# Kernel optimization log

Measured on AMD Instinct MI355X. Metric: run time of the kernel, lower is better.

## Reference

```python
import jax, jax.numpy as jnp
import numpy as np

B, D, LC, LQ = 64, 128, 1024, 128
NEG = -1e30


def setup_inputs() -> dict:
    key = jax.random.key(0)
    k1, k2, k3 = jax.random.split(key, 3)
    lim = float(np.sqrt(1.0 / D))
    return {
        "C": jax.random.normal(k1, (B, D, LC), dtype=jnp.float32),
        "Q": jax.random.normal(k2, (B, D, LQ), dtype=jnp.float32),
        "cmask": jnp.ones((B, LC), dtype=jnp.float32),
        "qmask": jnp.ones((B, LQ), dtype=jnp.float32),
        "w": jax.random.uniform(k3, (3 * D,), dtype=jnp.float32, minval=-lim, maxval=lim),
    }


def reference(C, Q, cmask, qmask, w):
    # C: [B, D, Lc], Q: [B, D, Lq] -> transpose to [B, L, D] as in the torch module
    Ct = jnp.swapaxes(C, 1, 2)  # [B, Lc, D]
    Qt = jnp.swapaxes(Q, 1, 2)  # [B, Lq, D]
    d = Ct.shape[-1]
    # Trilinear decomposition of the per-step concat([Qi, C, Q*C]) . w loop:
    # S[b,c,q] = Qt[b,q] . w_q + Ct[b,c] . w_c + (Ct[b,c] * w_m) . Qt[b,q]
    w_q, w_c, w_m = w[:d], w[d:2 * d], w[2 * d:]
    s_q = Qt @ w_q                                   # [B, Lq]
    s_c = Ct @ w_c                                   # [B, Lc]
    s_m = jnp.einsum("bcd,bqd->bcq", Ct * w_m, Qt)   # [B, Lc, Lq]
    S = s_m + s_c[:, :, None] + s_q[:, None, :]      # [B, Lc, Lq]

    S1 = jax.nn.softmax(S + (1.0 - qmask)[:, None, :] * NEG, axis=2)
    S2 = jax.nn.softmax(S + (1.0 - cmask)[:, :, None] * NEG, axis=1)

    A = jnp.einsum("bcq,bqd->bcd", S1, Qt)           # [B, Lc, D]
    S12 = jnp.einsum("bcq,bkq->bck", S1, S2)         # [B, Lc, Lc]
    Bt = jnp.einsum("bck,bkd->bcd", S12, Ct)         # [B, Lc, D]

    out = jnp.concatenate([Ct, A, Ct * A, Ct * Bt], axis=2)  # [B, Lc, 4D]
    # dropout is identity in eval mode
    return jnp.swapaxes(out, 1, 2)                   # [B, 4D, Lc]
```

## Files before the change

kernel.cpp:

```cpp
#include <hip/hip_runtime.h>
#include <cstdint>
#include <cstddef>

#define B_  64
#define D_  128
#define LC_ 1024
#define LQ_ 128
#define NEGV (-1e30f)
#define NINF (-3.402823466e38f)

typedef short s16x8 __attribute__((ext_vector_type(8)));
typedef float f32x4 __attribute__((ext_vector_type(4)));

__device__ __forceinline__ unsigned short f2bf(float x) {
    union { float f; unsigned u; } v; v.f = x;
    unsigned r = v.u + 0x7fffu + ((v.u >> 16) & 1u);
    return (unsigned short)(r >> 16);
}

__global__ __launch_bounds__(256, 2) void k1(const float* __restrict__ C,
                                             const float* __restrict__ Q,
                                             const float* __restrict__ cmask,
                                             const float* __restrict__ qmask,
                                             const float* __restrict__ w,
                                             unsigned short* __restrict__ S1b,
                                             float* __restrict__ pmax_g,
                                             float* __restrict__ psum_g,
                                             float* __restrict__ T2p) {
    __shared__ unsigned short CW[128 * 136];
    __shared__ unsigned short QT[128 * 136];
    __shared__ float4 red4[8][32];
    __shared__ float wc_l[128], wm_l[128], cmv_l[128], qmv_l[128], sc_l[128], sq_l[128];

    int t = threadIdx.x;
    int b = blockIdx.y, ct = blockIdx.x, c0 = ct * 128;
    int g = t >> 5, c4 = t & 31;

    float4 v[16];
    {
        const float4* Cb = (const float4*)(C + (size_t)b * D_ * LC_ + c0);
#pragma unroll
        for (int j = 0; j < 16; j++) {
            int d = j * 8 + g;
            v[j] = Cb[(size_t)d * (LC_ / 4) + c4];
        }
    }
    float* wq_l = (float*)red4;
    if (t < 128) {
        wq_l[t] = w[t];
        wc_l[t] = w[D_ + t];
        wm_l[t] = w[2 * D_ + t];
        cmv_l[t] = (1.0f - cmask[b * LC_ + c0 + t]) * NEGV;
        qmv_l[t] = (1.0f - qmask[b * LQ_ + t]) * NEGV;
    }
    __syncthreads();

    {
        float* CWf = (float*)CW;
        int qq = t >> 1, ph = t & 1;
        float sqv = 0.f;
#pragma unroll
        for (int h = 0; h < 2; h++) {
#pragma unroll
            for (int j = 0; j < 8; j++) {
                int idx = j * 256 + t;
                int r = idx >> 5, cc = idx & 31;
                float4 qv = *(const float4*)&Q[((size_t)(b * D_ + h * 64 + r)) * LQ_ + cc * 4];
                *(float4*)&CWf[r * 132 + cc * 4] = qv;
            }
            __syncthreads();
            unsigned short u[32];
#pragma unroll
            for (int k = 0; k < 32; k++) {
                float val = CWf[(ph * 32 + k) * 132 + qq];
                sqv += val * wq_l[h * 64 + ph * 32 + k];
                u[k] = f2bf(val);
            }
#pragma unroll
            for (int k4 = 0; k4 < 8; k4++) {
                ushort4 o;
                o.x = u[k4 * 4 + 0]; o.y = u[k4 * 4 + 1];
                o.z = u[k4 * 4 + 2]; o.w = u[k4 * 4 + 3];
                *(ushort4*)&QT[qq * 136 + h * 64 + ph * 32 + k4 * 4] = o;
            }
            __syncthreads();
        }
        sqv += __shfl_xor(sqv, 1, 64);
        if (ph == 0) sq_l[qq] = sqv;
    }

    {
        float4 scp = {0.f, 0.f, 0.f, 0.f};
#pragma unroll
        for (int j = 0; j < 16; j++) {
            int d = j * 8 + g;
            float wcv = wc_l[d], wmv = wm_l[d];
            scp.x += v[j].x * wcv;
            scp.y += v[j].y * wcv;
            scp.z += v[j].z * wcv;
            scp.w += v[j].w * wcv;
            ushort4 o;
            o.x = f2bf(v[j].x * wmv);
            o.y = f2bf(v[j].y * wmv);
            o.z = f2bf(v[j].z * wmv);
            o.w = f2bf(v[j].w * wmv);
            *(ushort4*)&CW[d * 136 + ((c4 ^ (j & 7)) << 2)] = o;
        }
        red4[g][c4] = scp;
    }
    __syncthreads();
    if (t < 128) {
        float s = 0.f;
#pragma unroll
        for (int gg = 0; gg < 8; gg++) {
            const float* rp = (const float*)&red4[gg][t >> 2];
            s += rp[t & 3];
        }
        sc_l[t] = s;
    }
    __syncthreads();

    int wv = t >> 6, l = t & 63, quad = l >> 4, lp = l & 15;
    int w32 = wv * 32;
    f32x4 zero = {0.f, 0.f, 0.f, 0.f};
    f32x4 acc[2][8];
#pragma unroll
    for (int mc = 0; mc < 2; mc++)
#pragma unroll
        for (int qt = 0; qt < 8; qt++) acc[mc][qt] = zero;

#pragma unroll
    for (int ks = 0; ks < 4; ks++) {
        s16x8 a[2], bb[8];
        int x3 = (ks * 4 + quad) & 7;
#pragma unroll
        for (int mc = 0; mc < 2; mc++) {
            s16x8 av;
            int c = w32 + mc * 16 + lp;
            int cb = ((c >> 2) ^ x3) << 2, clo = c & 3;
#pragma unroll
            for (int e = 0; e < 8; e++)
                av[e] = (short)CW[(ks * 32 + quad * 8 + e) * 136 + cb + clo];
            a[mc] = av;
        }
#pragma unroll
        for (int qt = 0; qt < 8; qt++)
            bb[qt] = *(const s16x8*)&QT[(qt * 16 + lp) * 136 + ks * 32 + quad * 8];
#pragma unroll
        for (int mc = 0; mc < 2; mc++)
#pragma unroll
            for (int qt = 0; qt < 8; qt++)
                acc[mc][qt] = __builtin_amdgcn_mfma_f32_16x16x32_bf16(a[mc], bb[qt], acc[mc][qt], 0, 0, 0);
    }
#pragma unroll
    for (int mc = 0; mc < 2; mc++)
#pragma unroll
        for (int qt = 0; qt < 8; qt++)
#pragma unroll
            for (int i = 0; i < 4; i++)
                acc[mc][qt][i] += sc_l[w32 + mc * 16 + quad * 4 + i] + sq_l[qt * 16 + lp];

    float qmv_r[8];
#pragma unroll
    for (int qt = 0; qt < 8; qt++) qmv_r[qt] = qmv_l[qt * 16 + lp];
    float cmv_r[2][4];
#pragma unroll
    for (int mc = 0; mc < 2; mc++)
#pragma unroll
        for (int i = 0; i < 4; i++) cmv_r[mc][i] = cmv_l[w32 + mc * 16 + quad * 4 + i];

    float rm_r[2][4];
#pragma unroll
    for (int mc = 0; mc < 2; mc++)
#pragma unroll
        for (int i = 0; i < 4; i++) {
            float m = NINF;
#pragma unroll
            for (int qt = 0; qt < 8; qt++) m = fmaxf(m, acc[mc][qt][i] + qmv_r[qt]);
#pragma unroll
            for (int off = 1; off < 16; off <<= 1) m = fmaxf(m, __shfl_xor(m, off, 64));
            rm_r[mc][i] = m;
        }

    int chunk = ct * 4 + wv;
#pragma unroll
    for (int qt = 0; qt < 8; qt++) {
        float cm = NINF;
#pragma unroll
        for (int mc = 0; mc < 2; mc++)
#pragma unroll
            for (int i = 0; i < 4; i++) cm = fmaxf(cm, acc[mc][qt][i] + cmv_r[mc][i]);
        cm = fmaxf(cm, __shfl_xor(cm, 16, 64));
        cm = fmaxf(cm, __shfl_xor(cm, 32, 64));
        float cs = 0.f;
#pragma unroll
        for (int mc = 0; mc < 2; mc++)
#pragma unroll
            for (int i = 0; i < 4; i++) cs += __expf(acc[mc][qt][i] + cmv_r[mc][i] - cm);
        cs += __shfl_xor(cs, 16, 64);
        cs += __shfl_xor(cs, 32, 64);
        if (l < 16) {
            pmax_g[((size_t)(b * 32 + chunk)) * LQ_ + qt * 16 + lp] = cm;
            psum_g[((size_t)(b * 32 + chunk)) * LQ_ + qt * 16 + lp] = cs;
        }
    }

    float ri_r[2][4], gs_r[2][4];
#pragma unroll
    for (int mc = 0; mc < 2; mc++)
#pragma unroll
        for (int i = 0; i < 4; i++) {
            float s = 0.f;
#pragma unroll
            for (int qt = 0; qt < 8; qt++) {
                float e = __expf(acc[mc][qt][i] + qmv_r[qt] - rm_r[mc][i]);
                acc[mc][qt][i] = e;
                s += e;
            }
#pragma unroll
            for (int off = 1; off < 16; off <<= 1) s += __shfl_xor(s, off, 64);
            ri_r[mc][i] = 1.0f / s;
            gs_r[mc][i] = s * __expf(rm_r[mc][i] + cmv_r[mc][i]);
        }

    __syncthreads();
#pragma unroll
    for (int mc = 0; mc < 2; mc++)
#pragma unroll
        for (int qt = 0; qt < 8; qt++)
#pragma unroll
            for (int i = 0; i < 4; i++) {
                int row = w32 + mc * 16 + quad * 4 + i;
                int q = qt * 16 + lp;
                float s1 = acc[mc][qt][i] * ri_r[mc][i];
                CW[row * 136 + q] = f2bf(s1);
                QT[q * 136 + row] = f2bf(s1 * gs_r[mc][i]);
            }
    __syncthreads();

    {
        int row = t >> 1, qh = (t & 1) * 64;
        const uint4* src = (const uint4*)&CW[row * 136 + qh];
        uint4* dst = (uint4*)&S1b[((size_t)(b * LC_ + c0 + row)) * LQ_ + qh];
#pragma unroll
        for (int j = 0; j < 8; j++) dst[j] = src[j];
    }

    f32x4 acc2[2][8];
#pragma unroll
    for (int mc = 0; mc < 2; mc++)
#pragma unroll
        for (int nt = 0; nt < 8; nt++) acc2[mc][nt] = zero;
#pragma unroll
    for (int ks = 0; ks < 4; ks++) {
        s16x8 a2[2], bb[8];
#pragma unroll
        for (int m = 0; m < 2; m++) {
            int d = w32 + m * 16 + lp;
            const float4* p = (const float4*)&C[((size_t)(b * D_ + d)) * LC_ + c0 + ks * 32 + quad * 8];
            float4 v0 = p[0], v1 = p[1];
            unsigned short* pp = (unsigned short*)&a2[m];
            pp[0] = f2bf(v0.x); pp[1] = f2bf(v0.y); pp[2] = f2bf(v0.z); pp[3] = f2bf(v0.w);
            pp[4] = f2bf(v1.x); pp[5] = f2bf(v1.y); pp[6] = f2bf(v1.z); pp[7] = f2bf(v1.w);
        }
#pragma unroll
        for (int nt = 0; nt < 8; nt++)
            bb[nt] = *(const s16x8*)&QT[(nt * 16 + lp) * 136 + ks * 32 + quad * 8];
#pragma unroll
        for (int m = 0; m < 2; m++)
#pragma unroll
            for (int nt = 0; nt < 8; nt++)
                acc2[m][nt] = __builtin_amdgcn_mfma_f32_16x16x32_bf16(a2[m], bb[nt], acc2[m][nt], 0, 0, 0);
    }
    size_t base = ((size_t)(ct * B_ + b)) * ((size_t)D_ * LQ_);
#pragma unroll
    for (int mc = 0; mc < 2; mc++)
#pragma unroll
        for (int i = 0; i < 4; i++) {
            int d = w32 + mc * 16 + quad * 4 + i;
#pragma unroll
            for (int nt = 0; nt < 8; nt++)
                T2p[base + (size_t)d * LQ_ + nt * 16 + lp] = acc2[mc][nt][i];
        }
}

__global__ __launch_bounds__(256) void k2(const float* __restrict__ pmax_g,
                                          const float* __restrict__ psum_g,
                                          const float* __restrict__ T2p,
                                          unsigned short* __restrict__ T2b) {
    __shared__ float scale_l[128];
    int t = threadIdx.x;
    int bid = blockIdx.x;
    int b = bid >> 3, dc = bid & 7;
    if (t < 128) {
        float m = NINF;
        for (int j = 0; j < 32; j++)
            m = fmaxf(m, pmax_g[((size_t)(b * 32 + j)) * LQ_ + t]);
        float s = 0.f;
        for (int j = 0; j < 32; j++)
            s += psum_g[((size_t)(b * 32 + j)) * LQ_ + t] *
                 __expf(pmax_g[((size_t)(b * 32 + j)) * LQ_ + t] - m);
        scale_l[t] = __expf(-m) / s;
    }
    __syncthreads();
    int d = dc * 16 + (t >> 4), q8 = (t & 15) * 8;
    float a8[8] = {0.f, 0.f, 0.f, 0.f, 0.f, 0.f, 0.f, 0.f};
#pragma unroll
    for (int j = 0; j < 8; j++) {
        const float* p = &T2p[(((size_t)j * B_ + b) * D_ + d) * LQ_ + q8];
        float4 x0 = *(const float4*)p, x1 = *(const float4*)(p + 4);
        a8[0] += x0.x; a8[1] += x0.y; a8[2] += x0.z; a8[3] += x0.w;
        a8[4] += x1.x; a8[5] += x1.y; a8[6] += x1.z; a8[7] += x1.w;
    }
    ushort4 o0, o1;
    o0.x = f2bf(a8[0] * scale_l[q8 + 0]);
    o0.y = f2bf(a8[1] * scale_l[q8 + 1]);
    o0.z = f2bf(a8[2] * scale_l[q8 + 2]);
    o0.w = f2bf(a8[3] * scale_l[q8 + 3]);
    o1.x = f2bf(a8[4] * scale_l[q8 + 4]);
    o1.y = f2bf(a8[5] * scale_l[q8 + 5]);
    o1.z = f2bf(a8[6] * scale_l[q8 + 6]);
    o1.w = f2bf(a8[7] * scale_l[q8 + 7]);
    size_t tb = ((size_t)(b * D_ + d)) * LQ_ + q8;
    *(ushort4*)&T2b[tb] = o0;
    *(ushort4*)&T2b[tb + 4] = o1;
}

__global__ __launch_bounds__(256) void k3(const float* __restrict__ C,
                                          const float* __restrict__ Q,
                                          const unsigned short* __restrict__ T2b,
                                          const unsigned short* __restrict__ S1b,
                                          float* __restrict__ out) {
    int t = threadIdx.x;
    int b = blockIdx.y, c0 = blockIdx.x * 128;
    int wv = t >> 6, l = t & 63, quad = l >> 4, lp = l & 15;
    int w32 = wv * 32;
    f32x4 zero = {0.f, 0.f, 0.f, 0.f};
    f32x4 accA[2][8], accB[2][8];
#pragma unroll
    for (int mc = 0; mc < 2; mc++)
#pragma unroll
        for (int nt = 0; nt < 8; nt++) { accA[mc][nt] = zero; accB[mc][nt] = zero; }

#pragma unroll
    for (int ks = 0; ks < 4; ks++) {
        s16x8 aq[2], at[2], bb[8];
#pragma unroll
        for (int mc = 0; mc < 2; mc++) {
            int d = w32 + mc * 16 + lp;
            const float4* p = (const float4*)&Q[((size_t)(b * D_ + d)) * LQ_ + ks * 32 + quad * 8];
            float4 v0 = p[0], v1 = p[1];
            unsigned short* pp = (unsigned short*)&aq[mc];
            pp[0] = f2bf(v0.x); pp[1] = f2bf(v0.y); pp[2] = f2bf(v0.z); pp[3] = f2bf(v0.w);
            pp[4] = f2bf(v1.x); pp[5] = f2bf(v1.y); pp[6] = f2bf(v1.z); pp[7] = f2bf(v1.w);
            at[mc] = *(const s16x8*)&T2b[((size_t)(b * D_ + d)) * LQ_ + ks * 32 + quad * 8];
        }
#pragma unroll
        for (int nt = 0; nt < 8; nt++)
            bb[nt] = *(const s16x8*)&S1b[((size_t)(b * LC_ + c0 + nt * 16 + lp)) * LQ_ + ks * 32 + quad * 8];
#pragma unroll
        for (int mc = 0; mc < 2; mc++)
#pragma unroll
            for (int nt = 0; nt < 8; nt++) {
                accA[mc][nt] = __builtin_amdgcn_mfma_f32_16x16x32_bf16(aq[mc], bb[nt], accA[mc][nt], 0, 0, 0);
                accB[mc][nt] = __builtin_amdgcn_mfma_f32_16x16x32_bf16(at[mc], bb[nt], accB[mc][nt], 0, 0, 0);
            }
    }
    const size_t DL = (size_t)D_ * LC_;
#pragma unroll
    for (int mc = 0; mc < 2; mc++)
#pragma unroll
        for (int i = 0; i < 4; i++) {
            int d = w32 + mc * 16 + quad * 4 + i;
            const float* Crow = C + ((size_t)(b * D_ + d)) * LC_ + c0;
            size_t ob = ((size_t)(b * 4 * D_ + d)) * LC_ + c0;
#pragma unroll
            for (int nt = 0; nt < 8; nt++) {
                int c = nt * 16 + lp;
                float cv = Crow[c];
                float a = accA[mc][nt][i];
                float bt = accB[mc][nt][i];
                out[ob + c] = cv;
                out[ob + DL + c] = a;
                out[ob + 2 * DL + c] = cv * a;
                out[ob + 3 * DL + c] = cv * bt;
            }
        }
}

extern "C" void kernel_launch(void* const* d_in, const int* in_sizes, int n_in,
                              void* d_out, int out_size, void* d_ws, size_t ws_size,
                              hipStream_t stream) {
    const float* C     = (const float*)d_in[0];
    const float* Q     = (const float*)d_in[1];
    const float* cmask = (const float*)d_in[2];
    const float* qmask = (const float*)d_in[3];
    const float* w     = (const float*)d_in[4];
    float* out = (float*)d_out;

    unsigned short* us = (unsigned short*)d_ws;
    unsigned short* S1b = us;
    unsigned short* T2b = S1b + (size_t)B_ * LC_ * LQ_;
    float* fp = (float*)(T2b + (size_t)B_ * D_ * LQ_);
    float* T2p    = fp;
    float* pmax_g = T2p + (size_t)8 * B_ * D_ * LQ_;
    float* psum_g = pmax_g + (size_t)B_ * 32 * LQ_;

    k1<<<dim3(LC_ / 128, B_), 256, 0, stream>>>(C, Q, cmask, qmask, w,
                                                S1b, pmax_g, psum_g, T2p);
    k2<<<dim3(B_ * 8), 256, 0, stream>>>(pmax_g, psum_g, T2p, T2b);
    k3<<<dim3(LC_ / 128, B_), 256, 0, stream>>>(C, Q, T2b, S1b, out);
}
```

Before: 219.1 us.

## Reuse LDS C*w_m tile for T2 partials, store partials in bf16, nontemporal output

The second GEMM in k1 now reads its C operand from the bf16 C*w_m tile already in shared memory (XOR-swizzled) and rescales the result by 1/w_m, instead of reloading and converting C from global memory. The S1 tile is kept in registers and written back to shared memory afterwards. T2 partials are stored as bf16 in a q-major layout, and k2 transposes them through shared memory, which halves the partial traffic. k3 uses nontemporal stores for the large output. The 1/w_m trick loses the contribution of any d where w_m is zero and adds bf16 rounding error.

```diff
diff --git a/kernel.cpp b/kernel.cpp
--- a/kernel.cpp
+++ b/kernel.cpp
@@ -16,6 +16,9 @@
     union { float f; unsigned u; } v; v.f = x;
     unsigned r = v.u + 0x7fffu + ((v.u >> 16) & 1u);
     return (unsigned short)(r >> 16);
+}
+__device__ __forceinline__ float bf2f(unsigned short u) {
+    union { unsigned u; float f; } v; v.u = ((unsigned)u) << 16; return v.f;
 }
 
 __global__ __launch_bounds__(256, 2) void k1(const float* __restrict__ C,
@@ -26,11 +29,11 @@
                                              unsigned short* __restrict__ S1b,
                                              float* __restrict__ pmax_g,
                                              float* __restrict__ psum_g,
-                                             float* __restrict__ T2p) {
+                                             unsigned short* __restrict__ T2pb) {
     __shared__ unsigned short CW[128 * 136];
     __shared__ unsigned short QT[128 * 136];
     __shared__ float4 red4[8][32];
-    __shared__ float wc_l[128], wm_l[128], cmv_l[128], qmv_l[128], sc_l[128], sq_l[128];
+    __shared__ float wc_l[128], wm_l[128], rwm_l[128], cmv_l[128], qmv_l[128], sc_l[128], sq_l[128];
 
     int t = threadIdx.x;
     int b = blockIdx.y, ct = blockIdx.x, c0 = ct * 128;
@@ -47,9 +50,11 @@
     }
     float* wq_l = (float*)red4;
     if (t < 128) {
+        float wmv = w[2 * D_ + t];
         wq_l[t] = w[t];
         wc_l[t] = w[D_ + t];
-        wm_l[t] = w[2 * D_ + t];
+        wm_l[t] = wmv;
+        rwm_l[t] = (wmv != 0.0f) ? (1.0f / wmv) : 0.0f;
         cmv_l[t] = (1.0f - cmask[b * LC_ + c0 + t]) * NEGV;
         qmv_l[t] = (1.0f - qmask[b * LQ_ + t]) * NEGV;
     }
@@ -223,21 +228,85 @@
             gs_r[mc][i] = s * __expf(rm_r[mc][i] + cmv_r[mc][i]);
         }
 
-    __syncthreads();
-#pragma unroll
-    for (int mc = 0; mc < 2; mc++)
-#pragma unroll
-        for (int qt = 0; qt < 8; qt++)
+    unsigned s1pk[2][8][2];
+    __syncthreads();
+#pragma unroll
+    for (int mc = 0; mc < 2; mc++)
+#pragma unroll
+        for (int qt = 0; qt < 8; qt++) {
+            unsigned short u[4];
 #pragma unroll
             for (int i = 0; i < 4; i++) {
                 int row = w32 + mc * 16 + quad * 4 + i;
                 int q = qt * 16 + lp;
                 float s1 = acc[mc][qt][i] * ri_r[mc][i];
-                CW[row * 136 + q] = f2bf(s1);
+                u[i] = f2bf(s1);
                 QT[q * 136 + row] = f2bf(s1 * gs_r[mc][i]);
             }
-    __syncthreads();
-
+            s1pk[mc][qt][0] = (unsigned)u[0] | ((unsigned)u[1] << 16);
+            s1pk[mc][qt][1] = (unsigned)u[2] | ((unsigned)u[3] << 16);
+        }
+    __syncthreads();
+
+    f32x4 acc2[2][8];
+#pragma unroll
+    for (int mc = 0; mc < 2; mc++)
+#pragma unroll
+        for (int nt = 0; nt < 8; nt++) acc2[mc][nt] = zero;
+#pragma unroll
+    for (int ks = 0; ks < 4; ks++) {
+        s16x8 a2[2], bb[8];
+#pragma unroll
+        for (int m = 0; m < 2; m++) {
+            int d = w32 + m * 16 + lp;
+            int xd = (d >> 3) & 7;
+            int cg = ks * 8 + quad * 2;
+            union { s16x8 vv; uint2 u2[2]; } A;
+            A.u2[0] = *(const uint2*)&CW[d * 136 + ((cg ^ xd) << 2)];
+            A.u2[1] = *(const uint2*)&CW[d * 136 + (((cg + 1) ^ xd) << 2)];
+            a2[m] = A.vv;
+        }
+#pragma unroll
+        for (int nt = 0; nt < 8; nt++)
+            bb[nt] = *(const s16x8*)&QT[(nt * 16 + lp) * 136 + ks * 32 + quad * 8];
+#pragma unroll
+        for (int m = 0; m < 2; m++)
+#pragma unroll
+            for (int nt = 0; nt < 8; nt++)
+                acc2[m][nt] = __builtin_amdgcn_mfma_f32_16x16x32_bf16(a2[m], bb[nt], acc2[m][nt], 0, 0, 0);
+    }
+    {
+        size_t baseq = ((size_t)(ct * B_ + b)) * LQ_;
+#pragma unroll
+        for (int mc = 0; mc < 2; mc++) {
+            int d0 = w32 + mc * 16 + quad * 4;
+            float r0 = rwm_l[d0], r1 = rwm_l[d0 + 1], r2 = rwm_l[d0 + 2], r3 = rwm_l[d0 + 3];
+#pragma unroll
+            for (int nt = 0; nt < 8; nt++) {
+                int q = nt * 16 + lp;
+                ushort4 o;
+                o.x = f2bf(acc2[mc][nt][0] * r0);
+                o.y = f2bf(acc2[mc][nt][1] * r1);
+                o.z = f2bf(acc2[mc][nt][2] * r2);
+                o.w = f2bf(acc2[mc][nt][3] * r3);
+                *(ushort4*)&T2pb[(baseq + q) * D_ + d0] = o;
+            }
+        }
+    }
+
+    __syncthreads();
+#pragma unroll
+    for (int mc = 0; mc < 2; mc++)
+#pragma unroll
+        for (int qt = 0; qt < 8; qt++) {
+            int row0 = w32 + mc * 16 + quad * 4;
+            int q = qt * 16 + lp;
+            CW[(row0 + 0) * 136 + q] = (unsigned short)(s1pk[mc][qt][0] & 0xffffu);
+            CW[(row0 + 1) * 136 + q] = (unsigned short)(s1pk[mc][qt][0] >> 16);
+            CW[(row0 + 2) * 136 + q] = (unsigned short)(s1pk[mc][qt][1] & 0xffffu);
+            CW[(row0 + 3) * 136 + q] = (unsigned short)(s1pk[mc][qt][1] >> 16);
+        }
+    __syncthreads();
     {
         int row = t >> 1, qh = (t & 1) * 64;
         const uint4* src = (const uint4*)&CW[row * 136 + qh];
@@ -245,50 +314,14 @@
 #pragma unroll
         for (int j = 0; j < 8; j++) dst[j] = src[j];
     }
-
-    f32x4 acc2[2][8];
-#pragma unroll
-    for (int mc = 0; mc < 2; mc++)
-#pragma unroll
-        for (int nt = 0; nt < 8; nt++) acc2[mc][nt] = zero;
-#pragma unroll
-    for (int ks = 0; ks < 4; ks++) {
-        s16x8 a2[2], bb[8];
-#pragma unroll
-        for (int m = 0; m < 2; m++) {
-            int d = w32 + m * 16 + lp;
-            const float4* p = (const float4*)&C[((size_t)(b * D_ + d)) * LC_ + c0 + ks * 32 + quad * 8];
-            float4 v0 = p[0], v1 = p[1];
-            unsigned short* pp = (unsigned short*)&a2[m];
-            pp[0] = f2bf(v0.x); pp[1] = f2bf(v0.y); pp[2] = f2bf(v0.z); pp[3] = f2bf(v0.w);
-            pp[4] = f2bf(v1.x); pp[5] = f2bf(v1.y); pp[6] = f2bf(v1.z); pp[7] = f2bf(v1.w);
-        }
-#pragma unroll
-        for (int nt = 0; nt < 8; nt++)
-            bb[nt] = *(const s16x8*)&QT[(nt * 16 + lp) * 136 + ks * 32 + quad * 8];
-#pragma unroll
-        for (int m = 0; m < 2; m++)
-#pragma unroll
-            for (int nt = 0; nt < 8; nt++)
-                acc2[m][nt] = __builtin_amdgcn_mfma_f32_16x16x32_bf16(a2[m], bb[nt], acc2[m][nt], 0, 0, 0);
-    }
-    size_t base = ((size_t)(ct * B_ + b)) * ((size_t)D_ * LQ_);
-#pragma unroll
-    for (int mc = 0; mc < 2; mc++)
-#pragma unroll
-        for (int i = 0; i < 4; i++) {
-            int d = w32 + mc * 16 + quad * 4 + i;
-#pragma unroll
-            for (int nt = 0; nt < 8; nt++)
-                T2p[base + (size_t)d * LQ_ + nt * 16 + lp] = acc2[mc][nt][i];
-        }
 }
 
 __global__ __launch_bounds__(256) void k2(const float* __restrict__ pmax_g,
                                           const float* __restrict__ psum_g,
-                                          const float* __restrict__ T2p,
+                                          const unsigned short* __restrict__ T2pb,
                                           unsigned short* __restrict__ T2b) {
     __shared__ float scale_l[128];
+    __shared__ float trans[16][132];
     int t = threadIdx.x;
     int bid = blockIdx.x;
     int b = bid >> 3, dc = bid & 7;
@@ -303,27 +336,32 @@
         scale_l[t] = __expf(-m) / s;
     }
     __syncthreads();
-    int d = dc * 16 + (t >> 4), q8 = (t & 15) * 8;
-    float a8[8] = {0.f, 0.f, 0.f, 0.f, 0.f, 0.f, 0.f, 0.f};
-#pragma unroll
-    for (int j = 0; j < 8; j++) {
-        const float* p = &T2p[(((size_t)j * B_ + b) * D_ + d) * LQ_ + q8];
-        float4 x0 = *(const float4*)p, x1 = *(const float4*)(p + 4);
-        a8[0] += x0.x; a8[1] += x0.y; a8[2] += x0.z; a8[3] += x0.w;
-        a8[4] += x1.x; a8[5] += x1.y; a8[6] += x1.z; a8[7] += x1.w;
-    }
-    ushort4 o0, o1;
-    o0.x = f2bf(a8[0] * scale_l[q8 + 0]);
-    o0.y = f2bf(a8[1] * scale_l[q8 + 1]);
-    o0.z = f2bf(a8[2] * scale_l[q8 + 2]);
-    o0.w = f2bf(a8[3] * scale_l[q8 + 3]);
-    o1.x = f2bf(a8[4] * scale_l[q8 + 4]);
-    o1.y = f2bf(a8[5] * scale_l[q8 + 5]);
-    o1.z = f2bf(a8[6] * scale_l[q8 + 6]);
-    o1.w = f2bf(a8[7] * scale_l[q8 + 7]);
-    size_t tb = ((size_t)(b * D_ + d)) * LQ_ + q8;
-    *(ushort4*)&T2b[tb] = o0;
-    *(ushort4*)&T2b[tb + 4] = o1;
+    {
+        int q = t >> 1, dh = t & 1;
+        float a8[8] = {0.f, 0.f, 0.f, 0.f, 0.f, 0.f, 0.f, 0.f};
+#pragma unroll
+        for (int j = 0; j < 8; j++) {
+            const ushort4* p = (const ushort4*)&T2pb[(((size_t)j * B_ + b) * LQ_ + q) * D_ + dc * 16 + dh * 8];
+            ushort4 x0 = p[0], x1 = p[1];
+            a8[0] += bf2f(x0.x); a8[1] += bf2f(x0.y); a8[2] += bf2f(x0.z); a8[3] += bf2f(x0.w);
+            a8[4] += bf2f(x1.x); a8[5] += bf2f(x1.y); a8[6] += bf2f(x1.z); a8[7] += bf2f(x1.w);
+        }
+        float sc = scale_l[q];
+#pragma unroll
+        for (int k = 0; k < 8; k++) trans[dh * 8 + k][q] = a8[k] * sc;
+    }
+    __syncthreads();
+    {
+        int dl = t >> 4, q8 = (t & 15) * 8;
+        f32x4 v0 = *(const f32x4*)&trans[dl][q8];
+        f32x4 v1 = *(const f32x4*)&trans[dl][q8 + 4];
+        ushort4 o0, o1;
+        o0.x = f2bf(v0[0]); o0.y = f2bf(v0[1]); o0.z = f2bf(v0[2]); o0.w = f2bf(v0[3]);
+        o1.x = f2bf(v1[0]); o1.y = f2bf(v1[1]); o1.z = f2bf(v1[2]); o1.w = f2bf(v1[3]);
+        size_t tb = ((size_t)(b * D_ + dc * 16 + dl)) * LQ_ + q8;
+        *(ushort4*)&T2b[tb] = o0;
+        *(ushort4*)&T2b[tb + 4] = o1;
+    }
 }
 
 __global__ __launch_bounds__(256) void k3(const float* __restrict__ C,
@@ -380,10 +418,10 @@
                 float cv = Crow[c];
                 float a = accA[mc][nt][i];
                 float bt = accB[mc][nt][i];
-                out[ob + c] = cv;
-                out[ob + DL + c] = a;
-                out[ob + 2 * DL + c] = cv * a;
-                out[ob + 3 * DL + c] = cv * bt;
+                __builtin_nontemporal_store(cv, &out[ob + c]);
+                __builtin_nontemporal_store(a, &out[ob + DL + c]);
+                __builtin_nontemporal_store(cv * a, &out[ob + 2 * DL + c]);
+                __builtin_nontemporal_store(cv * bt, &out[ob + 3 * DL + c]);
             }
         }
 }
@@ -399,15 +437,15 @@
     float* out = (float*)d_out;
 
     unsigned short* us = (unsigned short*)d_ws;
-    unsigned short* S1b = us;
-    unsigned short* T2b = S1b + (size_t)B_ * LC_ * LQ_;
-    float* fp = (float*)(T2b + (size_t)B_ * D_ * LQ_);
-    float* T2p    = fp;
-    float* pmax_g = T2p + (size_t)8 * B_ * D_ * LQ_;
+    unsigned short* S1b  = us;
+    unsigned short* T2b  = S1b + (size_t)B_ * LC_ * LQ_;
+    unsigned short* T2pb = T2b + (size_t)B_ * D_ * LQ_;
+    float* fp = (float*)(T2pb + (size_t)8 * B_ * D_ * LQ_);
+    float* pmax_g = fp;
     float* psum_g = pmax_g + (size_t)B_ * 32 * LQ_;
 
     k1<<<dim3(LC_ / 128, B_), 256, 0, stream>>>(C, Q, cmask, qmask, w,
-                                                S1b, pmax_g, psum_g, T2p);
-    k2<<<dim3(B_ * 8), 256, 0, stream>>>(pmax_g, psum_g, T2p, T2b);
+                                                S1b, pmax_g, psum_g, T2pb);
+    k2<<<dim3(B_ * 8), 256, 0, stream>>>(pmax_g, psum_g, T2pb, T2b);
     k3<<<dim3(LC_ / 128, B_), 256, 0, stream>>>(C, Q, T2b, S1b, out);
 }
```

Measured after the change: 235.5 us. 7.5% more time.
